# Optimization experiments

Measured on AMD Instinct MI355X. Metric: run time of the kernel, lower is better.

Reference implementation:

```python
import jax, jax.numpy as jnp
import numpy as np
from jax import lax


def _rnn_layer(x_tbd, h0, Wh, bh, Wo, bo):
    """Run one RNNBlock over time. x_tbd: [T,B,D], h0: [B,H]. Returns [T,B,out]."""
    def step(h, xt):
        c = jnp.concatenate([xt, h], axis=1)        # [B, D+H]
        h_new = jnp.tanh(c @ Wh + bh)               # [B, H]
        o = jnp.tanh(c @ Wo + bo)                   # [B, out]
        return h_new, o
    _, out = lax.scan(step, h0, x_tbd)
    return out


def setup_inputs() -> dict:
    key = jax.random.key(0)
    ks = jax.random.split(key, 10)
    B, T, D, H = 64, 256, 512, 512
    s = 0.03  # small init so tanh stays non-saturated
    return {
        "x": jax.random.normal(ks[0], (B, T, D), dtype=jnp.float32),
        "encoder_output": jax.random.normal(ks[1], (B, H), dtype=jnp.float32),
        "Wh0": jax.random.normal(ks[2], (D + H, H), dtype=jnp.float32) * s,
        "bh0": jax.random.normal(ks[3], (H,), dtype=jnp.float32) * s,
        "Wo0": jax.random.normal(ks[4], (D + H, D), dtype=jnp.float32) * s,
        "bo0": jax.random.normal(ks[5], (D,), dtype=jnp.float32) * s,
        "Wh1": jax.random.normal(ks[6], (D + H, H), dtype=jnp.float32) * s,
        "bh1": jax.random.normal(ks[7], (H,), dtype=jnp.float32) * s,
        "Wo1": jax.random.normal(ks[8], (D + H, D), dtype=jnp.float32) * s,
        "bo1": jax.random.normal(ks[9], (D,), dtype=jnp.float32) * s,
    }


def reference(x, encoder_output, Wh0, bh0, Wo0, bo0, Wh1, bh1, Wo1, bo1):
    B = x.shape[0]
    H1 = Wh1.shape[1]
    x_tbd = jnp.transpose(x, (1, 0, 2))                       # [T,B,D]
    # Layer 0: initial hidden = encoder_output
    out0 = _rnn_layer(x_tbd, encoder_output, Wh0, bh0, Wo0, bo0)
    # Layer 1: hidden reset to zeros (hidden=None in torch source)
    h0 = jnp.zeros((B, H1), dtype=x.dtype)
    out1 = _rnn_layer(out0, h0, Wh1, bh1, Wo1, bo1)
    return jnp.transpose(out1, (1, 0, 2))                     # [B,T,D]
```

## Files before the change

kernel.cpp:

```cpp
#include <hip/hip_runtime.h>
#include <hip/hip_bf16.h>
#include <hip/hip_fp16.h>

typedef unsigned int u32;
typedef unsigned short u16;
typedef short s16x8 __attribute__((ext_vector_type(8)));
typedef float f32x4 __attribute__((ext_vector_type(4)));
typedef _Float16 f16x2 __attribute__((ext_vector_type(2)));

#define T_STEPS 256

__device__ __forceinline__ u16 f2bu(float f) {
  return __bfloat16_as_ushort(__float2bfloat16(f));
}
__device__ __forceinline__ float fast_tanh(float x) {
  float ax = fabsf(x);
  float e = __expf(-2.f * ax);
  float r = 1.f - 2.f * e / (1.f + e);
  return copysignf(r, x);
}
__device__ __forceinline__ float fdot2u(u32 w, u32 h, float acc) {
#if __has_builtin(__builtin_amdgcn_fdot2)
  return __builtin_amdgcn_fdot2(__builtin_bit_cast(f16x2, w),
                                __builtin_bit_cast(f16x2, h), acc, false);
#else
  float w0 = __half2float(__ushort_as_half((u16)(w & 0xffff)));
  float w1 = __half2float(__ushort_as_half((u16)(w >> 16)));
  float g0 = __half2float(__ushort_as_half((u16)(h & 0xffff)));
  float g1 = __half2float(__ushort_as_half((u16)(h >> 16)));
  return acc + w0 * g0 + w1 * g1;
#endif
}
__device__ __forceinline__ void gload_lds16(const void* g, void* l) {
  __builtin_amdgcn_global_load_lds((const __attribute__((address_space(1))) u32*)g,
                                   (__attribute__((address_space(3))) u32*)l, 16, 0, 0);
}

__global__ void k_cvt_bf16(const float* __restrict__ in, u16* __restrict__ out, int n4) {
  int i = blockIdx.x * blockDim.x + threadIdx.x;
  if (i >= n4) return;
  const float4 v = ((const float4*)in)[i];
  ushort4 o;
  o.x = f2bu(v.x); o.y = f2bu(v.y); o.z = f2bu(v.z); o.w = f2bu(v.w);
  ((ushort4*)out)[i] = o;
}

__global__ void k_prep_w(const float* __restrict__ Wh, const float* __restrict__ Wo,
                         u16* __restrict__ BcatT, u16* __restrict__ WhoT,
                         u32* __restrict__ Wpack) {
  int idx = blockIdx.x * 256 + threadIdx.x;
  if (idx < 1024 * 512) {
    int n = idx >> 9, k = idx & 511;
    float v = (n < 512) ? Wh[k * 512 + n] : Wo[k * 512 + (n - 512)];
    BcatT[idx] = f2bu(v);
  } else if (idx < 1024 * 512 + 512 * 512) {
    int t = idx - 1024 * 512;
    int n = t >> 9, k = t & 511;
    WhoT[t] = f2bu(Wo[(512 + k) * 512 + n]);
  } else {
    int t = idx - (1024 * 512 + 512 * 512);
    int k2 = t >> 9, j = t & 511;
    u16 a = __half_as_ushort(__float2half(Wh[(512 + 2 * k2) * 512 + j]));
    u16 b = __half_as_ushort(__float2half(Wh[(512 + 2 * k2 + 1) * 512 + j]));
    Wpack[t] = (u32)a | ((u32)b << 16);
  }
}

template <int MODE>
__global__ __launch_bounds__(256) void k_gemm(
    const u16* __restrict__ A, const u16* __restrict__ BT, int NX,
    __half* __restrict__ outH, u16* __restrict__ outB, float* __restrict__ outF,
    const __half* __restrict__ Uo, const float* __restrict__ biasH,
    const float* __restrict__ biasO) {
  __shared__ __align__(16) u16 As[128 * 64], Bs[128 * 64];
  const int bid = blockIdx.x;
  const int bn = bid % NX, bm = bid / NX;
  const int m0 = bm * 128, n0 = bn * 128;
  const int tid = threadIdx.x, w = tid >> 6, l = tid & 63;
  const int l15 = l & 15, lk = (l >> 4) << 3;
  f32x4 acc[4][4] = {};
  for (int kt = 0; kt < 8; ++kt) {
    const int k0 = kt * 64;
#pragma unroll
    for (int i = 0; i < 4; ++i) {
      int idx = w * 4 + i;
      int ob = idx * 1024 + l * 16;
      int row = ob >> 7, cb = ob & 127;
      int scb = cb ^ ((row & 7) << 4);
      gload_lds16((const char*)A + (size_t)(m0 + row) * 1024 + k0 * 2 + scb,
                  (char*)As + idx * 1024);
      gload_lds16((const char*)BT + (size_t)(n0 + row) * 1024 + k0 * 2 + scb,
                  (char*)Bs + idx * 1024);
    }
    __syncthreads();
    const int wr = (w >> 1) * 64, wc = (w & 1) * 64;
#pragma unroll
    for (int kk = 0; kk < 2; ++kk) {
      s16x8 af[4], bfr[4];
      const int kb = (kk * 32 + lk) * 2;
#pragma unroll
      for (int i = 0; i < 4; ++i) {
        int ar = wr + i * 16 + l15;
        af[i] = *(const s16x8*)((const char*)As + ar * 128 + (kb ^ ((ar & 7) << 4)));
        int br = wc + i * 16 + l15;
        bfr[i] = *(const s16x8*)((const char*)Bs + br * 128 + (kb ^ ((br & 7) << 4)));
      }
#pragma unroll
      for (int i = 0; i < 4; ++i)
#pragma unroll
        for (int jj = 0; jj < 4; ++jj)
          acc[i][jj] = __builtin_amdgcn_mfma_f32_16x16x32_bf16(af[i], bfr[jj], acc[i][jj], 0, 0, 0);
    }
    __syncthreads();
  }
#pragma unroll
  for (int i = 0; i < 4; ++i)
#pragma unroll
    for (int jj = 0; jj < 4; ++jj)
#pragma unroll
      for (int rr = 0; rr < 4; ++rr) {
        int row = m0 + (w >> 1) * 64 + i * 16 + ((l >> 4) << 2) + rr;
        int col = n0 + (w & 1) * 64 + jj * 16 + l15;
        float v = acc[i][jj][rr];
        if (MODE == 0) {
          float bsv = (col < 512) ? biasH[col] : biasO[col - 512];
          outH[(size_t)row * 1024 + col] = __float2half(v + bsv);
        } else {
          float o = fast_tanh(v + __half2float(Uo[(size_t)row * 1024 + col]));
          if (MODE == 1) outB[(size_t)row * 512 + col] = f2bu(o);
          else           outF[(size_t)row * 512 + col] = o;
        }
      }
}

#define REG_G 48
#define LDS_G 7
#define STR_G 9

__global__ __launch_bounds__(512, 2) void k_scan(
    const u32* __restrict__ Wpack, const __half* __restrict__ Uh,
    const float* __restrict__ h0, u16* __restrict__ Hseq) {
  __shared__ u32 Wlds[LDS_G * 4 * 512];
  __shared__ __align__(16) __half hbuf[512];
  const int b = blockIdx.x, j = threadIdx.x;
  u32 wreg[REG_G * 4];
#pragma unroll
  for (int p = 0; p < REG_G * 4; ++p) wreg[p] = Wpack[p * 512 + j];
#pragma unroll
  for (int p = 0; p < LDS_G * 4; ++p) Wlds[p * 512 + j] = Wpack[(REG_G * 4 + p) * 512 + j];
  float h = h0 ? h0[b * 512 + j] : 0.f;
  hbuf[j] = __float2half(h);
  __syncthreads();
  const uint4* h4 = (const uint4*)hbuf;
  int r = b * T_STEPS;
  for (int t = 0; t < T_STEPS; ++t, ++r) {
    u32 wst[STR_G * 4];
#pragma unroll
    for (int p = 0; p < STR_G * 4; ++p)
      wst[p] = Wpack[((REG_G + LDS_G) * 4 + p) * 512 + j];
    float acc = __half2float(Uh[r * 1024 + j]);
    Hseq[r * 512 + j] = f2bu(h);
#pragma unroll
    for (int g = 0; g < REG_G; ++g) {
      uint4 hv = h4[g];
      acc = fdot2u(wreg[4 * g + 0], hv.x, acc);
      acc = fdot2u(wreg[4 * g + 1], hv.y, acc);
      acc = fdot2u(wreg[4 * g + 2], hv.z, acc);
      acc = fdot2u(wreg[4 * g + 3], hv.w, acc);
    }
#pragma unroll
    for (int g = 0; g < LDS_G; ++g) {
      uint4 hv = h4[REG_G + g];
      acc = fdot2u(Wlds[(4 * g + 0) * 512 + j], hv.x, acc);
      acc = fdot2u(Wlds[(4 * g + 1) * 512 + j], hv.y, acc);
      acc = fdot2u(Wlds[(4 * g + 2) * 512 + j], hv.z, acc);
      acc = fdot2u(Wlds[(4 * g + 3) * 512 + j], hv.w, acc);
    }
#pragma unroll
    for (int g = 0; g < STR_G; ++g) {
      uint4 hv = h4[REG_G + LDS_G + g];
      acc = fdot2u(wst[4 * g + 0], hv.x, acc);
      acc = fdot2u(wst[4 * g + 1], hv.y, acc);
      acc = fdot2u(wst[4 * g + 2], hv.z, acc);
      acc = fdot2u(wst[4 * g + 3], hv.w, acc);
    }
    float hn = fast_tanh(acc);
    __syncthreads();
    hbuf[j] = __float2half(hn);
    h = hn;
    __syncthreads();
  }
}

extern "C" void kernel_launch(void* const* d_in, const int* in_sizes, int n_in,
                              void* d_out, int out_size, void* d_ws, size_t ws_size,
                              hipStream_t stream) {
  const float* x   = (const float*)d_in[0];
  const float* enc = (const float*)d_in[1];
  const float* Wh0 = (const float*)d_in[2];
  const float* bh0 = (const float*)d_in[3];
  const float* Wo0 = (const float*)d_in[4];
  const float* bo0 = (const float*)d_in[5];
  const float* Wh1 = (const float*)d_in[6];
  const float* bh1 = (const float*)d_in[7];
  const float* Wo1 = (const float*)d_in[8];
  const float* bo1 = (const float*)d_in[9];
  char* ws = (char*)d_ws;
  u16*    Xbf   = (u16*)(ws);
  __half* U     = (__half*)(ws + 16777216);
  u16*    Hs0   = (u16*)(ws + 16777216 + 33554432);
  u16*    Out0  = (u16*)(ws + 16777216 + 33554432 + 16777216);
  u16*    Hs1   = (u16*)(ws + 16777216 + 33554432 + 2 * 16777216);
  char*   wb    = ws + 16777216 + 33554432 + 3 * 16777216;
  u16*    Bct0  = (u16*)(wb);
  u16*    WhoT0 = (u16*)(wb + 1048576);
  u32*    Wpk0  = (u32*)(wb + 1048576 + 524288);
  u16*    Bct1  = (u16*)(wb + 1048576 + 2 * 524288);
  u16*    WhoT1 = (u16*)(wb + 2 * 1048576 + 2 * 524288);
  u32*    Wpk1  = (u32*)(wb + 2 * 1048576 + 3 * 524288);

  k_cvt_bf16<<<8192, 256, 0, stream>>>(x, Xbf, 8388608 / 4);
  k_prep_w<<<3584, 256, 0, stream>>>(Wh0, Wo0, Bct0, WhoT0, Wpk0);
  k_prep_w<<<3584, 256, 0, stream>>>(Wh1, Wo1, Bct1, WhoT1, Wpk1);
  k_gemm<0><<<1024, 256, 0, stream>>>(Xbf, Bct0, 8, U, nullptr, nullptr, nullptr, bh0, bo0);
  k_scan<<<64, 512, 0, stream>>>(Wpk0, U, enc, Hs0);
  k_gemm<1><<<512, 256, 0, stream>>>(Hs0, WhoT0, 4, nullptr, Out0, nullptr, U + 512, nullptr, nullptr);
  k_gemm<0><<<1024, 256, 0, stream>>>(Out0, Bct1, 8, U, nullptr, nullptr, nullptr, bh1, bo1);
  k_scan<<<64, 512, 0, stream>>>(Wpk1, U, nullptr, Hs1);
  k_gemm<2><<<512, 256, 0, stream>>>(Hs1, WhoT1, 4, nullptr, nullptr, (float*)d_out, U + 512, nullptr, nullptr);
}
```

Before: 1.099 ms.

## Keep all scan weights on-chip, double-buffer hidden state, prefetch U input

The recurrent scan kernel no longer streams part of the weight matrix from global memory every timestep. It keeps 184 packed words per thread in registers and the remaining 72 in 144KB of dynamic LDS, laid out so each thread reads them with 16-byte vector loads. The hidden-state buffer is double-buffered, which removes one of the two barriers per step, and the next step's U value is prefetched one step ahead. This relies on large dynamic LDS and a waves-per-EU attribute, so register spills or occupancy limits are the risk.

```diff
diff --git a/kernel.cpp b/kernel.cpp
--- a/kernel.cpp
+++ b/kernel.cpp
@@ -133,35 +133,38 @@
       }
 }
 
-#define REG_G 48
-#define LDS_G 7
-#define STR_G 9
-
-__global__ __launch_bounds__(512, 2) void k_scan(
-    const u32* __restrict__ Wpack, const __half* __restrict__ Uh,
-    const float* __restrict__ h0, u16* __restrict__ Hseq) {
-  __shared__ u32 Wlds[LDS_G * 4 * 512];
-  __shared__ __align__(16) __half hbuf[512];
+#define REG_P 184
+#define LDS_GRP 18
+#define SCAN_LDS_BYTES (LDS_GRP * 2048 * 4 + 2048)
+
+__global__ __launch_bounds__(512) __attribute__((amdgpu_waves_per_eu(2, 2)))
+void k_scan(const u32* __restrict__ Wpack, const __half* __restrict__ Uh,
+            const float* __restrict__ h0, u16* __restrict__ Hseq) {
+  extern __shared__ __align__(16) u32 smem[];
+  u32* Wl = smem;
+  __half* hb = (__half*)(smem + LDS_GRP * 2048);
   const int b = blockIdx.x, j = threadIdx.x;
-  u32 wreg[REG_G * 4];
-#pragma unroll
-  for (int p = 0; p < REG_G * 4; ++p) wreg[p] = Wpack[p * 512 + j];
-#pragma unroll
-  for (int p = 0; p < LDS_G * 4; ++p) Wlds[p * 512 + j] = Wpack[(REG_G * 4 + p) * 512 + j];
+  u32 wreg[REG_P];
+#pragma unroll
+  for (int p = 0; p < REG_P; ++p) wreg[p] = Wpack[p * 512 + j];
+  for (int g = 0; g < LDS_GRP; ++g)
+#pragma unroll
+    for (int q = 0; q < 4; ++q)
+      Wl[g * 2048 + j * 4 + q] = Wpack[(REG_P + 4 * g + q) * 512 + j];
   float h = h0 ? h0[b * 512 + j] : 0.f;
-  hbuf[j] = __float2half(h);
+  hb[j] = __float2half(h);
   __syncthreads();
-  const uint4* h4 = (const uint4*)hbuf;
-  int r = b * T_STEPS;
-  for (int t = 0; t < T_STEPS; ++t, ++r) {
-    u32 wst[STR_G * 4];
-#pragma unroll
-    for (int p = 0; p < STR_G * 4; ++p)
-      wst[p] = Wpack[((REG_G + LDS_G) * 4 + p) * 512 + j];
-    float acc = __half2float(Uh[r * 1024 + j]);
-    Hseq[r * 512 + j] = f2bu(h);
-#pragma unroll
-    for (int g = 0; g < REG_G; ++g) {
+  const int r0 = b * T_STEPS;
+  float u_cur = __half2float(Uh[(size_t)r0 * 1024 + j]);
+  for (int t = 0; t < T_STEPS; ++t) {
+    const int r = r0 + t;
+    const int rn = (t < T_STEPS - 1) ? r + 1 : r;
+    float u_nxt = __half2float(Uh[(size_t)rn * 1024 + j]);
+    Hseq[(size_t)r * 512 + j] = f2bu(h);
+    const uint4* h4 = (const uint4*)(hb + (t & 1) * 512);
+    float acc = u_cur;
+#pragma unroll
+    for (int g = 0; g < 46; ++g) {
       uint4 hv = h4[g];
       acc = fdot2u(wreg[4 * g + 0], hv.x, acc);
       acc = fdot2u(wreg[4 * g + 1], hv.y, acc);
@@ -169,25 +172,18 @@
       acc = fdot2u(wreg[4 * g + 3], hv.w, acc);
     }
 #pragma unroll
-    for (int g = 0; g < LDS_G; ++g) {
-      uint4 hv = h4[REG_G + g];
-      acc = fdot2u(Wlds[(4 * g + 0) * 512 + j], hv.x, acc);
-      acc = fdot2u(Wlds[(4 * g + 1) * 512 + j], hv.y, acc);
-      acc = fdot2u(Wlds[(4 * g + 2) * 512 + j], hv.z, acc);
-      acc = fdot2u(Wlds[(4 * g + 3) * 512 + j], hv.w, acc);
-    }
-#pragma unroll
-    for (int g = 0; g < STR_G; ++g) {
-      uint4 hv = h4[REG_G + LDS_G + g];
-      acc = fdot2u(wst[4 * g + 0], hv.x, acc);
-      acc = fdot2u(wst[4 * g + 1], hv.y, acc);
-      acc = fdot2u(wst[4 * g + 2], hv.z, acc);
-      acc = fdot2u(wst[4 * g + 3], hv.w, acc);
+    for (int g = 0; g < LDS_GRP; ++g) {
+      uint4 hv = h4[46 + g];
+      uint4 wv = *(const uint4*)&Wl[g * 2048 + j * 4];
+      acc = fdot2u(wv.x, hv.x, acc);
+      acc = fdot2u(wv.y, hv.y, acc);
+      acc = fdot2u(wv.z, hv.z, acc);
+      acc = fdot2u(wv.w, hv.w, acc);
     }
     float hn = fast_tanh(acc);
-    __syncthreads();
-    hbuf[j] = __float2half(hn);
+    hb[((t + 1) & 1) * 512 + j] = __float2half(hn);
     h = hn;
+    u_cur = u_nxt;
     __syncthreads();
   }
 }
@@ -219,13 +215,17 @@
   u16*    WhoT1 = (u16*)(wb + 2 * 1048576 + 2 * 524288);
   u32*    Wpk1  = (u32*)(wb + 2 * 1048576 + 3 * 524288);
 
+  (void)hipFuncSetAttribute((const void*)k_scan,
+                            hipFuncAttributeMaxDynamicSharedMemorySize,
+                            SCAN_LDS_BYTES);
+
   k_cvt_bf16<<<8192, 256, 0, stream>>>(x, Xbf, 8388608 / 4);
   k_prep_w<<<3584, 256, 0, stream>>>(Wh0, Wo0, Bct0, WhoT0, Wpk0);
   k_prep_w<<<3584, 256, 0, stream>>>(Wh1, Wo1, Bct1, WhoT1, Wpk1);
   k_gemm<0><<<1024, 256, 0, stream>>>(Xbf, Bct0, 8, U, nullptr, nullptr, nullptr, bh0, bo0);
-  k_scan<<<64, 512, 0, stream>>>(Wpk0, U, enc, Hs0);
+  k_scan<<<64, 512, SCAN_LDS_BYTES, stream>>>(Wpk0, U, enc, Hs0);
   k_gemm<1><<<512, 256, 0, stream>>>(Hs0, WhoT0, 4, nullptr, Out0, nullptr, U + 512, nullptr, nullptr);
   k_gemm<0><<<1024, 256, 0, stream>>>(Out0, Bct1, 8, U, nullptr, nullptr, nullptr, bh1, bo1);
-  k_scan<<<64, 512, 0, stream>>>(Wpk1, U, nullptr, Hs1);
+  k_scan<<<64, 512, SCAN_LDS_BYTES, stream>>>(Wpk1, U, nullptr, Hs1);
   k_gemm<2><<<512, 256, 0, stream>>>(Hs1, WhoT1, 4, nullptr, nullptr, (float*)d_out, U + 512, nullptr, nullptr);
 }
```

Result: faster. 1.048 ms (-4.6%).
